# Optimization experiments

Hardware: AMD Instinct MI355X
Metric: run time of the kernel (lower is better)

Reference implementation:

```python
import jax, jax.numpy as jnp
import numpy as np

GRID_SIZE = 5
SPLINE_ORDER = 3
NUM_EXPERTS = 8
TOP_K = 2
CAP_FACTOR = 1.25
TEMP = 1.0
GDHW = (4, 4, 4)


def make_grid(in_features):
    # efficient-KAN grid buffer: grid_range=[-1,1], extended by spline_order on each side
    h = 2.0 / GRID_SIZE
    g = jnp.arange(-SPLINE_ORDER, GRID_SIZE + SPLINE_ORDER + 1, dtype=jnp.float32) * h - 1.0
    return jnp.broadcast_to(g, (in_features, g.shape[0]))


def b_splines(x, grid):
    # x: (N, in) -> (N, in, GRID_SIZE + SPLINE_ORDER) Cox-de Boor bases
    x = x[:, :, None]
    bases = ((x >= grid[:, :-1]) & (x < grid[:, 1:])).astype(x.dtype)
    for k in range(1, SPLINE_ORDER + 1):
        left = (x - grid[:, : -(k + 1)]) / (grid[:, k:-1] - grid[:, : -(k + 1)])
        right = (grid[:, k + 1:] - x) / (grid[:, k + 1:] - grid[:, 1:-k])
        bases = left * bases[:, :, :-1] + right * bases[:, :, 1:]
    return bases


def kan_linear(x, base_w, spline_w, scaler, grid):
    base = jax.nn.silu(x) @ base_w.T
    bs = b_splines(x, grid)                                   # (N, in, coef)
    spline = jnp.einsum('nic,oic->no', bs, spline_w * scaler[:, :, None])
    return base + spline


def layernorm(x, w, b, eps=1e-5):
    mu = x.mean(-1, keepdims=True)
    var = x.var(-1, keepdims=True)
    return (x - mu) / jnp.sqrt(var + eps) * w + b


def setup_inputs() -> dict:
    key = jax.random.key(0)
    ks = jax.random.split(key, 12)
    Cf, hidden, E, nc = 256, 170, NUM_EXPERTS, 2
    coef = GRID_SIZE + SPLINE_ORDER
    def nrm(k, shape, scale):
        return jax.random.normal(k, shape, dtype=jnp.float32) * scale
    return {
        'fpn_feat': nrm(ks[0], (8, 254, 32, 32, 32), 1.0),
        'seg_logits': nrm(ks[1], (8, 2, 32, 32, 32), 1.0),
        'ln_r_w': jnp.ones((Cf,), jnp.float32),
        'ln_r_b': jnp.zeros((Cf,), jnp.float32),
        'ln_h_w': jnp.ones((Cf,), jnp.float32),
        'ln_h_b': jnp.zeros((Cf,), jnp.float32),
        'router_w': nrm(ks[2], (E, Cf), Cf ** -0.5),
        'router_b': jnp.zeros((E,), jnp.float32),
        'bw1': nrm(ks[3], (E, hidden, Cf), Cf ** -0.5),
        'sw1': nrm(ks[4], (E, hidden, Cf, coef), 0.1 * Cf ** -0.5),
        'sc1': nrm(ks[5], (E, hidden, Cf), Cf ** -0.5),
        'bw2': nrm(ks[6], (E, Cf, hidden), hidden ** -0.5),
        'sw2': nrm(ks[7], (E, Cf, hidden, coef), 0.1 * hidden ** -0.5),
        'sc2': nrm(ks[8], (E, Cf, hidden), hidden ** -0.5),
        'cls_bw': nrm(ks[9], (nc, Cf), Cf ** -0.5),
        'cls_sw': nrm(ks[10], (nc, Cf, coef), 0.1 * Cf ** -0.5),
        'cls_sc': nrm(ks[11], (nc, Cf), Cf ** -0.5),
        'grid_cf': make_grid(Cf),
        'grid_hid': make_grid(hidden),
    }


def reference(fpn_feat, seg_logits, ln_r_w, ln_r_b, ln_h_w, ln_h_b,
              router_w, router_b, bw1, sw1, sc1, bw2, sw2, sc2,
              cls_bw, cls_sw, cls_sc, grid_cf, grid_hid):
    fused = jnp.concatenate([fpn_feat, seg_logits], axis=1)   # (B, Cf, D, H, W)
    B, C, D, H, W = fused.shape
    gd, gh, gw = GDHW
    dp, hp, wp = D // gd, H // gh, W // gw
    # split into gd*gh*gw blocks per sample
    blk = fused.reshape(B, C, gd, dp, gh, hp, gw, wp)
    blk = blk.transpose(0, 2, 4, 6, 1, 3, 5, 7).reshape(-1, C, dp, hp, wp)
    vec = blk.mean(axis=(2, 3, 4))                            # (N, Cf) global avg pool

    N = vec.shape[0]
    E = NUM_EXPERTS
    x_norm = layernorm(vec, ln_r_w, ln_r_b)
    scores = (x_norm @ router_w.T + router_b) / TEMP          # (N, E)
    top_val, top_idx = jax.lax.top_k(scores, TOP_K)
    top_w = jax.nn.softmax(top_val, axis=-1)
    capacity = int(CAP_FACTOR * N * TOP_K / E) + 1

    onehot = top_idx[None] == jnp.arange(E)[:, None, None]    # (E, N, K)
    sel = onehot.any(-1)                                      # (E, N)
    pos = jnp.cumsum(sel.astype(jnp.int32), axis=1)           # rank among selected (1-based)
    keep = sel & (pos <= capacity)                            # capacity drop = first-come order
    w = (top_w[None] * onehot.astype(top_w.dtype)).sum(-1)    # (E, N) combine weights

    def expert(bw1e, sw1e, sc1e, bw2e, sw2e, sc2e):
        h = kan_linear(x_norm, bw1e, sw1e, sc1e, grid_cf)
        h = jax.nn.gelu(h, approximate=False)                 # torch nn.GELU default (erf)
        return kan_linear(h, bw2e, sw2e, sc2e, grid_hid)

    y_all = jax.vmap(expert)(bw1, sw1, sc1, bw2, sw2, sc2)    # (E, N, Cf)
    out = jnp.einsum('en,enc->nc', keep.astype(vec.dtype) * w, y_all)

    conf = scores.max(-1)                                     # (N,)
    logits_blk = kan_linear(layernorm(out, ln_h_w, ln_h_b), cls_bw, cls_sw, cls_sc, grid_cf)
    P = gd * gh * gw
    weight = jax.nn.softmax(conf.reshape(B, P), axis=-1)[:, :, None]
    logits = (logits_blk.reshape(B, P, -1) * weight).sum(1)   # (B, num_classes)
    return logits
```

## Files before the change

kernel.cpp:

```cpp
#include <hip/hip_runtime.h>
#include <math.h>

#define CF 256
#define HID 170
#define NE 8
#define NTOK 512
#define K1 2304
#define K2P 1536
#define CAPACITY 161

typedef __bf16 bf16x8 __attribute__((ext_vector_type(8)));
typedef unsigned short u16x8 __attribute__((ext_vector_type(8)));
typedef float f32x4 __attribute__((ext_vector_type(4)));

__device__ __forceinline__ float silu_f(float x) { return x / (1.0f + expf(-x)); }
__device__ __forceinline__ float gelu_f(float x) {
    return 0.5f * x * (1.0f + erff(x * 0.70710678118654752f));
}

__device__ __forceinline__ unsigned short f2bf(float f) {
    unsigned int u = __float_as_uint(f);
    u = u + 0x7fffu + ((u >> 16) & 1u);
    return (unsigned short)(u >> 16);
}

__device__ __forceinline__ void bspline8(float x, float bs[8]) {
    float b[11];
#pragma unroll
    for (int j = 0; j < 11; ++j) {
        float g0 = (float)(j - 3) * 0.4f - 1.0f;
        float g1 = (float)(j - 2) * 0.4f - 1.0f;
        b[j] = (x >= g0 && x < g1) ? 1.0f : 0.0f;
    }
#pragma unroll
    for (int k = 1; k <= 3; ++k) {
        float inv = 2.5f / (float)k;
#pragma unroll
        for (int j = 0; j < 10 - (k - 1); ++j) {
            float gj   = (float)(j - 3) * 0.4f - 1.0f;
            float gjk1 = (float)(j - 2 + k) * 0.4f - 1.0f;
            b[j] = (x - gj) * inv * b[j] + (gjk1 - x) * inv * b[j + 1];
        }
    }
#pragma unroll
    for (int c = 0; c < 8; ++c) bs[c] = b[c];
}

__global__ __launch_bounds__(256) void mega_front_kernel(const float* __restrict__ fpn,
                                                         const float* __restrict__ seg,
                                                         const float* __restrict__ bw1,
                                                         const float* __restrict__ sw1,
                                                         const float* __restrict__ sc1,
                                                         const float* __restrict__ bw2,
                                                         const float* __restrict__ sw2,
                                                         const float* __restrict__ sc2,
                                                         float* __restrict__ vec,
                                                         unsigned short* __restrict__ W1,
                                                         unsigned short* __restrict__ W2) {
    int id = blockIdx.x, tid = threadIdx.x;
    if (id < 2048) {
        int c = id & 255, b = id >> 8;
        const float* src = (c < 254) ? fpn + (size_t)(b * 254 + c) * 32768
                                     : seg + (size_t)(b * 2 + (c - 254)) * 32768;
        const float4* s4 = (const float4*)src;
        float s[4] = {0.f, 0.f, 0.f, 0.f};
#pragma unroll
        for (int it = 0; it < 32; ++it) {
            float4 v = s4[it * 256 + tid];
            s[it >> 3] += v.x + v.y + v.z + v.w;
        }
        __shared__ float acc[64];
        if (tid < 64) acc[tid] = 0.0f;
        __syncthreads();
        int bh = tid >> 6, bw = (tid & 7) >> 1;
#pragma unroll
        for (int bd = 0; bd < 4; ++bd) atomicAdd(&acc[bd * 16 + bh * 4 + bw], s[bd]);
        __syncthreads();
        if (tid < 64) vec[(size_t)(b * 64 + tid) * CF + c] = acc[tid] * (1.0f / 512.0f);
    } else if (id < 2048 + NE * HID) {
        int r = id - 2048;
        int o = r % HID, e = r / HID, i = tid;
        size_t oi = (size_t)(e * HID + o) * CF + i;
        unsigned short* row = W1 + (size_t)(e * HID + o) * K1;
        row[i] = f2bf(bw1[oi]);
        float sc = sc1[oi];
        const float* sw = sw1 + oi * 8;
        u16x8 pk;
#pragma unroll
        for (int c = 0; c < 8; ++c) pk[c] = f2bf(sw[c] * sc);
        *(u16x8*)(row + CF + i * 8) = pk;
    } else {
        int r = id - (2048 + NE * HID);
        int o = r & 255, e = r >> 8, t = tid;
        unsigned short* row = W2 + (size_t)(e * CF + o) * K2P;
        if (t < HID) {
            size_t oi = (size_t)(e * CF + o) * HID + t;
            row[t] = f2bf(bw2[oi]);
            float sc = sc2[oi];
            const float* sw = sw2 + oi * 8;
            u16x8 pk;
#pragma unroll
            for (int c = 0; c < 8; ++c) pk[c] = f2bf(sw[c] * sc);
            *(u16x8*)(row + HID + t * 8) = pk;
        } else if (t < HID + 6) {
            row[HID * 9 + (t - HID)] = 0;
        }
    }
}

__global__ __launch_bounds__(256) void ln_score_a1_kernel(const float* __restrict__ vec,
                                                          const float* __restrict__ lnw,
                                                          const float* __restrict__ lnb,
                                                          const float* __restrict__ rw,
                                                          const float* __restrict__ rb,
                                                          float* __restrict__ scores,
                                                          unsigned short* __restrict__ A1) {
    int n = blockIdx.x, i = threadIdx.x;
    float v = vec[(size_t)n * CF + i];
    float s1 = v, s2 = v * v;
#pragma unroll
    for (int off = 32; off > 0; off >>= 1) {
        s1 += __shfl_xor(s1, off);
        s2 += __shfl_xor(s2, off);
    }
    __shared__ float rs1[4], rs2[4];
    int lane = i & 63, wid = i >> 6;
    if (lane == 0) { rs1[wid] = s1; rs2[wid] = s2; }
    __syncthreads();
    float tot1 = rs1[0] + rs1[1] + rs1[2] + rs1[3];
    float tot2 = rs2[0] + rs2[1] + rs2[2] + rs2[3];
    float mu = tot1 * (1.0f / CF);
    float var = tot2 * (1.0f / CF) - mu * mu;
    float rsd = rsqrtf(var + 1e-5f);
    float xv = (v - mu) * rsd * lnw[i] + lnb[i];
    unsigned short* r = A1 + (size_t)n * K1;
    r[i] = f2bf(silu_f(xv));
    float bs[8]; bspline8(xv, bs);
    u16x8 pk;
#pragma unroll
    for (int c = 0; c < 8; ++c) pk[c] = f2bf(bs[c]);
    *(u16x8*)(r + CF + i * 8) = pk;
    float p[NE];
#pragma unroll
    for (int e = 0; e < NE; ++e) p[e] = xv * rw[e * CF + i];
#pragma unroll
    for (int off = 32; off > 0; off >>= 1)
#pragma unroll
        for (int e = 0; e < NE; ++e) p[e] += __shfl_xor(p[e], off);
    __shared__ float pacc[4][NE];
    if (lane == 0)
#pragma unroll
        for (int e = 0; e < NE; ++e) pacc[wid][e] = p[e];
    __syncthreads();
    if (i < NE)
        scores[n * NE + i] = pacc[0][i] + pacc[1][i] + pacc[2][i] + pacc[3][i] + rb[i];
}

__global__ __launch_bounds__(512) void topk_kernel(const float* __restrict__ scores,
                                                   float* __restrict__ cw,
                                                   float* __restrict__ conf) {
    int n = threadIdx.x;
    __shared__ int   ti0[NTOK], ti1[NTOK];
    __shared__ float tw0[NTOK], tw1[NTOK];
    float m1 = -1e30f, m2 = -1e30f; int i1 = 0, i2 = 0;
#pragma unroll
    for (int e = 0; e < NE; ++e) {
        float sc = scores[n * NE + e];
        if (sc > m1) { m2 = m1; i2 = i1; m1 = sc; i1 = e; }
        else if (sc > m2) { m2 = sc; i2 = e; }
    }
    conf[n] = m1;
    float ew = expf(m2 - m1);
    ti0[n] = i1; ti1[n] = i2;
    tw0[n] = 1.0f / (1.0f + ew); tw1[n] = ew / (1.0f + ew);
    __syncthreads();
    int e = n >> 6, lane = n & 63;
    int cnt = 0;
    for (int c = 0; c < NTOK / 64; ++c) {
        int t = c * 64 + lane;
        int h0 = (ti0[t] == e), h1 = (ti1[t] == e);
        int sel = h0 | h1;
        unsigned long long mask = __ballot(sel);
        int pos = cnt + (int)__popcll(mask & ((1ull << lane) - 1ull));
        float wv = 0.f;
        if (sel && pos < CAPACITY) wv = h0 ? tw0[t] : tw1[t];
        cw[e * NTOK + t] = wv;
        cnt += (int)__popcll(mask);
    }
}

__global__ __launch_bounds__(256) void gemm_mfma_kernel(const unsigned short* __restrict__ Ag,
                                                        const unsigned short* __restrict__ Bg,
                                                        float* __restrict__ C,
                                                        unsigned short* __restrict__ A2,
                                                        int N, int K, long sA, long sB, long sC,
                                                        int ldc, int mode) {
    int e = blockIdx.z;
    const unsigned short* A = Ag + (size_t)e * sA;
    const unsigned short* B = Bg + (size_t)e * sB;
    int m0 = blockIdx.y * 64, n0 = blockIdx.x * 64;

    __shared__ alignas(16) unsigned char AsB[8192];
    __shared__ alignas(16) unsigned char BsB[8192];

    int tid = threadIdx.x;
    int lane = tid & 63, w = tid >> 6;
    int wr = w >> 1, wc = w & 1;
    int fr = lane & 15, fg = lane >> 4;
    int srow = tid >> 3;
    int schunk = tid & 7;

    int r0 = srow, r1 = srow + 32;
    int wb0 = r0 * 128 + ((schunk * 16) ^ ((r0 & 7) << 4));
    int wb1 = r1 * 128 + ((schunk * 16) ^ ((r1 & 7) << 4));

    f32x4 acc[2][2];
#pragma unroll
    for (int i = 0; i < 2; ++i)
#pragma unroll
        for (int j = 0; j < 2; ++j)
#pragma unroll
            for (int r = 0; r < 4; ++r) acc[i][j][r] = 0.f;

    int bn0 = n0 + r0, bn1 = n0 + r1;
    const int steps = K >> 6;
    u16x8 a0, a1, b0, b1;
    a0 = *(const u16x8*)(A + (size_t)(m0 + r0) * K + schunk * 8);
    a1 = *(const u16x8*)(A + (size_t)(m0 + r1) * K + schunk * 8);
    b0 = b1 = (u16x8){0, 0, 0, 0, 0, 0, 0, 0};
    if (bn0 < N) b0 = *(const u16x8*)(B + (size_t)bn0 * K + schunk * 8);
    if (bn1 < N) b1 = *(const u16x8*)(B + (size_t)bn1 * K + schunk * 8);

    for (int s = 0; s < steps; ++s) {
        __syncthreads();
        *(u16x8*)(AsB + wb0) = a0;
        *(u16x8*)(AsB + wb1) = a1;
        *(u16x8*)(BsB + wb0) = b0;
        *(u16x8*)(BsB + wb1) = b1;
        __syncthreads();
        if (s + 1 < steps) {
            int k0 = (s + 1) << 6;
            a0 = *(const u16x8*)(A + (size_t)(m0 + r0) * K + k0 + schunk * 8);
            a1 = *(const u16x8*)(A + (size_t)(m0 + r1) * K + k0 + schunk * 8);
            if (bn0 < N) b0 = *(const u16x8*)(B + (size_t)bn0 * K + k0 + schunk * 8);
            if (bn1 < N) b1 = *(const u16x8*)(B + (size_t)bn1 * K + k0 + schunk * 8);
        }
#pragma unroll
        for (int ks = 0; ks < 2; ++ks) {
            int kb = ks * 64 + fg * 16;
            u16x8 af[2], bf[2];
#pragma unroll
            for (int mf = 0; mf < 2; ++mf) {
                int row = wr * 32 + mf * 16 + fr;
                af[mf] = *(const u16x8*)(AsB + row * 128 + (kb ^ ((row & 7) << 4)));
            }
#pragma unroll
            for (int nf = 0; nf < 2; ++nf) {
                int row = wc * 32 + nf * 16 + fr;
                bf[nf] = *(const u16x8*)(BsB + row * 128 + (kb ^ ((row & 7) << 4)));
            }
#pragma unroll
            for (int mf = 0; mf < 2; ++mf)
#pragma unroll
                for (int nf = 0; nf < 2; ++nf)
                    acc[mf][nf] = __builtin_amdgcn_mfma_f32_16x16x32_bf16(
                        __builtin_bit_cast(bf16x8, af[mf]),
                        __builtin_bit_cast(bf16x8, bf[nf]), acc[mf][nf], 0, 0, 0);
        }
    }

    if (mode == 1) {
#pragma unroll
        for (int mf = 0; mf < 2; ++mf)
#pragma unroll
            for (int nf = 0; nf < 2; ++nf)
#pragma unroll
                for (int r = 0; r < 4; ++r) {
                    int row = m0 + wr * 32 + mf * 16 + fg * 4 + r;
                    int col = n0 + wc * 32 + nf * 16 + fr;
                    if (col < N) {
                        float g = gelu_f(acc[mf][nf][r]);
                        unsigned short* rr = A2 + ((size_t)e * NTOK + row) * K2P;
                        rr[col] = f2bf(silu_f(g));
                        float bs[8]; bspline8(g, bs);
                        u16x8 pk;
#pragma unroll
                        for (int c = 0; c < 8; ++c) pk[c] = f2bf(bs[c]);
                        *(u16x8*)(rr + HID + col * 8) = pk;
                    }
                }
    } else {
        float* Ce = C + (size_t)e * sC;
#pragma unroll
        for (int mf = 0; mf < 2; ++mf)
#pragma unroll
            for (int nf = 0; nf < 2; ++nf)
#pragma unroll
                for (int r = 0; r < 4; ++r) {
                    int row = m0 + wr * 32 + mf * 16 + fg * 4 + r;
                    int col = n0 + wc * 32 + nf * 16 + fr;
                    if (col < N) Ce[(size_t)row * ldc + col] = acc[mf][nf][r];
                }
    }
}

__global__ __launch_bounds__(256) void combcls_kernel(const float* __restrict__ y,
                                                      const float* __restrict__ cw,
                                                      const float* __restrict__ lnw,
                                                      const float* __restrict__ lnb,
                                                      const float* __restrict__ cbw,
                                                      const float* __restrict__ csw,
                                                      const float* __restrict__ csc,
                                                      float* __restrict__ lblk) {
    int n = blockIdx.x, i = threadIdx.x;
    float v = 0.f;
#pragma unroll
    for (int e = 0; e < NE; ++e)
        v += cw[e * NTOK + n] * y[((size_t)(e * NTOK + n)) * CF + i];
    float s1 = v, s2 = v * v;
#pragma unroll
    for (int off = 32; off > 0; off >>= 1) {
        s1 += __shfl_xor(s1, off);
        s2 += __shfl_xor(s2, off);
    }
    __shared__ float rA[4], rB[4], rP0[4], rP1[4];
    int lane = i & 63, wid = i >> 6;
    if (lane == 0) { rA[wid] = s1; rB[wid] = s2; }
    __syncthreads();
    float tot1 = rA[0] + rA[1] + rA[2] + rA[3];
    float tot2 = rB[0] + rB[1] + rB[2] + rB[3];
    float mu = tot1 * (1.0f / CF);
    float var = tot2 * (1.0f / CF) - mu * mu;
    float rs = rsqrtf(var + 1e-5f);
    float xh = (v - mu) * rs * lnw[i] + lnb[i];
    float si = silu_f(xh);
    float bs[8]; bspline8(xh, bs);
    float p0 = si * cbw[i], p1 = si * cbw[CF + i];
    float sp0 = 0.f, sp1 = 0.f;
#pragma unroll
    for (int c = 0; c < 8; ++c) {
        sp0 += bs[c] * csw[(size_t)i * 8 + c];
        sp1 += bs[c] * csw[(size_t)(CF + i) * 8 + c];
    }
    p0 += sp0 * csc[i];
    p1 += sp1 * csc[CF + i];
#pragma unroll
    for (int off = 32; off > 0; off >>= 1) {
        p0 += __shfl_xor(p0, off);
        p1 += __shfl_xor(p1, off);
    }
    if (lane == 0) { rP0[wid] = p0; rP1[wid] = p1; }
    __syncthreads();
    if (i == 0) {
        lblk[n * 2 + 0] = rP0[0] + rP0[1] + rP0[2] + rP0[3];
        lblk[n * 2 + 1] = rP1[0] + rP1[1] + rP1[2] + rP1[3];
    }
}

__global__ __launch_bounds__(64) void final_kernel(const float* __restrict__ conf,
                                                   const float* __restrict__ lblk,
                                                   float* __restrict__ out) {
    int b = blockIdx.x, p = threadIdx.x;
    float cf = conf[b * 64 + p];
    float mx = cf;
#pragma unroll
    for (int off = 32; off > 0; off >>= 1) mx = fmaxf(mx, __shfl_xor(mx, off));
    float ev = expf(cf - mx);
    float s = ev;
#pragma unroll
    for (int off = 32; off > 0; off >>= 1) s += __shfl_xor(s, off);
    float w = ev / s;
    float l0 = w * lblk[(b * 64 + p) * 2 + 0];
    float l1 = w * lblk[(b * 64 + p) * 2 + 1];
#pragma unroll
    for (int off = 32; off > 0; off >>= 1) {
        l0 += __shfl_xor(l0, off);
        l1 += __shfl_xor(l1, off);
    }
    if (p == 0) { out[b * 2 + 0] = l0; out[b * 2 + 1] = l1; }
}

extern "C" void kernel_launch(void* const* d_in, const int* in_sizes, int n_in,
                              void* d_out, int out_size, void* d_ws, size_t ws_size,
                              hipStream_t stream) {
    const float* fpn      = (const float*)d_in[0];
    const float* seg      = (const float*)d_in[1];
    const float* ln_r_w   = (const float*)d_in[2];
    const float* ln_r_b   = (const float*)d_in[3];
    const float* ln_h_w   = (const float*)d_in[4];
    const float* ln_h_b   = (const float*)d_in[5];
    const float* router_w = (const float*)d_in[6];
    const float* router_b = (const float*)d_in[7];
    const float* bw1      = (const float*)d_in[8];
    const float* sw1      = (const float*)d_in[9];
    const float* sc1      = (const float*)d_in[10];
    const float* bw2      = (const float*)d_in[11];
    const float* sw2      = (const float*)d_in[12];
    const float* sc2      = (const float*)d_in[13];
    const float* cls_bw   = (const float*)d_in[14];
    const float* cls_sw   = (const float*)d_in[15];
    const float* cls_sc   = (const float*)d_in[16];

    float* ws = (float*)d_ws;
    float* vec    = ws;
    float* scores = vec + 131072;
    float* cw     = scores + 4096;
    float* conf   = cw + 4096;
    float* lblk   = conf + 512;
    float* yall   = lblk + 1024;
    unsigned short* A1b = (unsigned short*)(yall + 1048576);
    unsigned short* W1b = A1b + (size_t)NTOK * K1;
    unsigned short* A2b = W1b + (size_t)NE * HID * K1;
    unsigned short* W2b = A2b + (size_t)NE * NTOK * K2P;

    mega_front_kernel<<<dim3(2048 + NE * HID + 2048), dim3(256), 0, stream>>>(
        fpn, seg, bw1, sw1, sc1, bw2, sw2, sc2, vec, W1b, W2b);
    ln_score_a1_kernel<<<dim3(NTOK), dim3(256), 0, stream>>>(vec, ln_r_w, ln_r_b, router_w,
                                                             router_b, scores, A1b);
    topk_kernel<<<dim3(1), dim3(512), 0, stream>>>(scores, cw, conf);
    gemm_mfma_kernel<<<dim3(3, 8, NE), dim3(256), 0, stream>>>(
        A1b, W1b, nullptr, A2b, HID, K1, 0L, (long)HID * K1, 0L, 0, 1);
    gemm_mfma_kernel<<<dim3(4, 8, NE), dim3(256), 0, stream>>>(
        A2b, W2b, yall, nullptr, CF, K2P, (long)NTOK * K2P, (long)CF * K2P,
        (long)NTOK * CF, CF, 0);
    combcls_kernel<<<dim3(NTOK), dim3(256), 0, stream>>>(yall, cw, ln_h_w, ln_h_b, cls_bw,
                                                         cls_sw, cls_sc, lblk);
    final_kernel<<<dim3(8), dim3(64), 0, stream>>>(conf, lblk, (float*)d_out);
}
```

Measured before the change: 117.1 us.

## Use direct global-to-LDS double-buffered loads in GEMM and fuse small kernels

The GEMM mainloop now stages tiles with global_load_lds into double-buffered shared memory, waiting on vmcnt, instead of loading through registers and storing to LDS. The top-k routing kernel is folded into an extra block of the first GEMM launch, and the final softmax-weighted reduction moves into combcls using atomicAdd into an output zeroed by the front kernel. This removes two launches and register staging, at the cost of atomic ordering nondeterminism and the removal of the N-bound guard on B loads, which now reads rows beyond N into padded tiles.

```diff
diff --git a/kernel.cpp b/kernel.cpp
--- a/kernel.cpp
+++ b/kernel.cpp
@@ -22,6 +22,12 @@
     unsigned int u = __float_as_uint(f);
     u = u + 0x7fffu + ((u >> 16) & 1u);
     return (unsigned short)(u >> 16);
+}
+
+__device__ __forceinline__ void gl_lds16(const unsigned short* g, unsigned short* l) {
+    __builtin_amdgcn_global_load_lds(
+        (const __attribute__((address_space(1))) unsigned int*)g,
+        (__attribute__((address_space(3))) unsigned int*)l, 16, 0, 0);
 }
 
 __device__ __forceinline__ void bspline8(float x, float bs[8]) {
@@ -56,8 +62,10 @@
                                                          const float* __restrict__ sc2,
                                                          float* __restrict__ vec,
                                                          unsigned short* __restrict__ W1,
-                                                         unsigned short* __restrict__ W2) {
+                                                         unsigned short* __restrict__ W2,
+                                                         float* __restrict__ out) {
     int id = blockIdx.x, tid = threadIdx.x;
+    if (id == 2048 && tid < 16) out[tid] = 0.0f;
     if (id < 2048) {
         int c = id & 255, b = id >> 8;
         const float* src = (c < 254) ? fpn + (size_t)(b * 254 + c) * 32768
@@ -114,8 +122,13 @@
                                                           const float* __restrict__ rw,
                                                           const float* __restrict__ rb,
                                                           float* __restrict__ scores,
-                                                          unsigned short* __restrict__ A1) {
+                                                          unsigned short* __restrict__ A1,
+                                                          unsigned short* __restrict__ A2) {
     int n = blockIdx.x, i = threadIdx.x;
+    if (i < 48) {
+        int e = i / 6, j = i - e * 6;
+        A2[((size_t)e * NTOK + n) * K2P + HID * 9 + j] = 0;
+    }
     float v = vec[(size_t)n * CF + i];
     float s1 = v, s2 = v * v;
 #pragma unroll
@@ -156,63 +169,80 @@
         scores[n * NE + i] = pacc[0][i] + pacc[1][i] + pacc[2][i] + pacc[3][i] + rb[i];
 }
 
-__global__ __launch_bounds__(512) void topk_kernel(const float* __restrict__ scores,
-                                                   float* __restrict__ cw,
-                                                   float* __restrict__ conf) {
-    int n = threadIdx.x;
+__global__ __launch_bounds__(256) void gemm_mfma_kernel(
+        const unsigned short* __restrict__ Ag, const unsigned short* __restrict__ Bg,
+        float* __restrict__ C, unsigned short* __restrict__ A2,
+        const float* __restrict__ scores, float* __restrict__ cw, float* __restrict__ conf,
+        int N, int K, long sA, long sB, long sC, int ldc, int mode) {
+    __shared__ alignas(16) unsigned short As[2][4096];
+    __shared__ alignas(16) unsigned short Bs[2][4096];
     __shared__ int   ti0[NTOK], ti1[NTOK];
     __shared__ float tw0[NTOK], tw1[NTOK];
-    float m1 = -1e30f, m2 = -1e30f; int i1 = 0, i2 = 0;
-#pragma unroll
-    for (int e = 0; e < NE; ++e) {
-        float sc = scores[n * NE + e];
-        if (sc > m1) { m2 = m1; i2 = i1; m1 = sc; i1 = e; }
-        else if (sc > m2) { m2 = sc; i2 = e; }
-    }
-    conf[n] = m1;
-    float ew = expf(m2 - m1);
-    ti0[n] = i1; ti1[n] = i2;
-    tw0[n] = 1.0f / (1.0f + ew); tw1[n] = ew / (1.0f + ew);
-    __syncthreads();
-    int e = n >> 6, lane = n & 63;
-    int cnt = 0;
-    for (int c = 0; c < NTOK / 64; ++c) {
-        int t = c * 64 + lane;
-        int h0 = (ti0[t] == e), h1 = (ti1[t] == e);
-        int sel = h0 | h1;
-        unsigned long long mask = __ballot(sel);
-        int pos = cnt + (int)__popcll(mask & ((1ull << lane) - 1ull));
-        float wv = 0.f;
-        if (sel && pos < CAPACITY) wv = h0 ? tw0[t] : tw1[t];
-        cw[e * NTOK + t] = wv;
-        cnt += (int)__popcll(mask);
-    }
-}
-
-__global__ __launch_bounds__(256) void gemm_mfma_kernel(const unsigned short* __restrict__ Ag,
-                                                        const unsigned short* __restrict__ Bg,
-                                                        float* __restrict__ C,
-                                                        unsigned short* __restrict__ A2,
-                                                        int N, int K, long sA, long sB, long sC,
-                                                        int ldc, int mode) {
+
+    int tid = threadIdx.x;
+    if (mode == 1 && blockIdx.x == 3) {
+        if (blockIdx.y != 0 || blockIdx.z != 0) return;
+        int lane = tid & 63, w4 = tid >> 6;
+#pragma unroll
+        for (int half = 0; half < 2; ++half) {
+            int n = half * 256 + tid;
+            float m1 = -1e30f, m2 = -1e30f; int i1 = 0, i2 = 0;
+#pragma unroll
+            for (int e = 0; e < NE; ++e) {
+                float sc = scores[n * NE + e];
+                if (sc > m1) { m2 = m1; i2 = i1; m1 = sc; i1 = e; }
+                else if (sc > m2) { m2 = sc; i2 = e; }
+            }
+            conf[n] = m1;
+            float ew = expf(m2 - m1);
+            ti0[n] = i1; ti1[n] = i2;
+            tw0[n] = 1.0f / (1.0f + ew); tw1[n] = ew / (1.0f + ew);
+        }
+        __syncthreads();
+#pragma unroll
+        for (int e2 = 0; e2 < 2; ++e2) {
+            int e = w4 * 2 + e2;
+            int cnt = 0;
+#pragma unroll
+            for (int c = 0; c < NTOK / 64; ++c) {
+                int t = c * 64 + lane;
+                int h0 = (ti0[t] == e), h1 = (ti1[t] == e);
+                int sel = h0 | h1;
+                unsigned long long mask = __ballot(sel);
+                int pos = cnt + (int)__popcll(mask & ((1ull << lane) - 1ull));
+                float wv = 0.f;
+                if (sel && pos < CAPACITY) wv = h0 ? tw0[t] : tw1[t];
+                cw[e * NTOK + t] = wv;
+                cnt += (int)__popcll(mask);
+            }
+        }
+        return;
+    }
+
     int e = blockIdx.z;
     const unsigned short* A = Ag + (size_t)e * sA;
     const unsigned short* B = Bg + (size_t)e * sB;
     int m0 = blockIdx.y * 64, n0 = blockIdx.x * 64;
-
-    __shared__ alignas(16) unsigned char AsB[8192];
-    __shared__ alignas(16) unsigned char BsB[8192];
-
-    int tid = threadIdx.x;
     int lane = tid & 63, w = tid >> 6;
     int wr = w >> 1, wc = w & 1;
     int fr = lane & 15, fg = lane >> 4;
-    int srow = tid >> 3;
-    int schunk = tid & 7;
-
-    int r0 = srow, r1 = srow + 32;
-    int wb0 = r0 * 128 + ((schunk * 16) ^ ((r0 & 7) << 4));
-    int wb1 = r1 * 128 + ((schunk * 16) ^ ((r1 & 7) << 4));
+    int lrow = lane >> 3, lch = lane & 7;
+    int csw = (lch ^ lrow) * 8;
+
+    const unsigned short* aS0 = A + (size_t)(m0 + w * 16 + lrow) * K + csw;
+    const unsigned short* aS1 = aS0 + (size_t)8 * K;
+    const unsigned short* bS0 = B + (size_t)(n0 + w * 16 + lrow) * K + csw;
+    const unsigned short* bS1 = bS0 + (size_t)8 * K;
+    unsigned short* dA0[2] = {&As[0][(w * 16) * 64], &As[1][(w * 16) * 64]};
+    unsigned short* dA1[2] = {&As[0][(w * 16 + 8) * 64], &As[1][(w * 16 + 8) * 64]};
+    unsigned short* dB0[2] = {&Bs[0][(w * 16) * 64], &Bs[1][(w * 16) * 64]};
+    unsigned short* dB1[2] = {&Bs[0][(w * 16 + 8) * 64], &Bs[1][(w * 16 + 8) * 64]};
+
+#define STAGE(bi, k0)                 \
+    gl_lds16(aS0 + (k0), dA0[bi]);    \
+    gl_lds16(aS1 + (k0), dA1[bi]);    \
+    gl_lds16(bS0 + (k0), dB0[bi]);    \
+    gl_lds16(bS1 + (k0), dB1[bi]);
 
     f32x4 acc[2][2];
 #pragma unroll
@@ -222,29 +252,20 @@
 #pragma unroll
             for (int r = 0; r < 4; ++r) acc[i][j][r] = 0.f;
 
-    int bn0 = n0 + r0, bn1 = n0 + r1;
     const int steps = K >> 6;
-    u16x8 a0, a1, b0, b1;
-    a0 = *(const u16x8*)(A + (size_t)(m0 + r0) * K + schunk * 8);
-    a1 = *(const u16x8*)(A + (size_t)(m0 + r1) * K + schunk * 8);
-    b0 = b1 = (u16x8){0, 0, 0, 0, 0, 0, 0, 0};
-    if (bn0 < N) b0 = *(const u16x8*)(B + (size_t)bn0 * K + schunk * 8);
-    if (bn1 < N) b1 = *(const u16x8*)(B + (size_t)bn1 * K + schunk * 8);
-
+    STAGE(0, 0);
     for (int s = 0; s < steps; ++s) {
-        __syncthreads();
-        *(u16x8*)(AsB + wb0) = a0;
-        *(u16x8*)(AsB + wb1) = a1;
-        *(u16x8*)(BsB + wb0) = b0;
-        *(u16x8*)(BsB + wb1) = b1;
-        __syncthreads();
+        int bi = s & 1;
         if (s + 1 < steps) {
-            int k0 = (s + 1) << 6;
-            a0 = *(const u16x8*)(A + (size_t)(m0 + r0) * K + k0 + schunk * 8);
-            a1 = *(const u16x8*)(A + (size_t)(m0 + r1) * K + k0 + schunk * 8);
-            if (bn0 < N) b0 = *(const u16x8*)(B + (size_t)bn0 * K + k0 + schunk * 8);
-            if (bn1 < N) b1 = *(const u16x8*)(B + (size_t)bn1 * K + k0 + schunk * 8);
-        }
+            STAGE(bi ^ 1, (s + 1) << 6);
+            asm volatile("s_waitcnt vmcnt(4)" ::: "memory");
+        } else {
+            asm volatile("s_waitcnt vmcnt(0)" ::: "memory");
+        }
+        __builtin_amdgcn_s_barrier();
+        asm volatile("" ::: "memory");
+        const unsigned char* Ab = (const unsigned char*)As[bi];
+        const unsigned char* Bb = (const unsigned char*)Bs[bi];
 #pragma unroll
         for (int ks = 0; ks < 2; ++ks) {
             int kb = ks * 64 + fg * 16;
@@ -252,12 +273,12 @@
 #pragma unroll
             for (int mf = 0; mf < 2; ++mf) {
                 int row = wr * 32 + mf * 16 + fr;
-                af[mf] = *(const u16x8*)(AsB + row * 128 + (kb ^ ((row & 7) << 4)));
+                af[mf] = *(const u16x8*)(Ab + row * 128 + (kb ^ ((row & 7) << 4)));
             }
 #pragma unroll
             for (int nf = 0; nf < 2; ++nf) {
                 int row = wc * 32 + nf * 16 + fr;
-                bf[nf] = *(const u16x8*)(BsB + row * 128 + (kb ^ ((row & 7) << 4)));
+                bf[nf] = *(const u16x8*)(Bb + row * 128 + (kb ^ ((row & 7) << 4)));
             }
 #pragma unroll
             for (int mf = 0; mf < 2; ++mf)
@@ -267,7 +288,11 @@
                         __builtin_bit_cast(bf16x8, af[mf]),
                         __builtin_bit_cast(bf16x8, bf[nf]), acc[mf][nf], 0, 0, 0);
         }
-    }
+        asm volatile("" ::: "memory");
+        __builtin_amdgcn_s_barrier();
+        asm volatile("" ::: "memory");
+    }
+#undef STAGE
 
     if (mode == 1) {
 #pragma unroll
@@ -306,12 +331,13 @@
 
 __global__ __launch_bounds__(256) void combcls_kernel(const float* __restrict__ y,
                                                       const float* __restrict__ cw,
+                                                      const float* __restrict__ conf,
                                                       const float* __restrict__ lnw,
                                                       const float* __restrict__ lnb,
                                                       const float* __restrict__ cbw,
                                                       const float* __restrict__ csw,
                                                       const float* __restrict__ csc,
-                                                      float* __restrict__ lblk) {
+                                                      float* __restrict__ out) {
     int n = blockIdx.x, i = threadIdx.x;
     float v = 0.f;
 #pragma unroll
@@ -351,33 +377,24 @@
     }
     if (lane == 0) { rP0[wid] = p0; rP1[wid] = p1; }
     __syncthreads();
-    if (i == 0) {
-        lblk[n * 2 + 0] = rP0[0] + rP0[1] + rP0[2] + rP0[3];
-        lblk[n * 2 + 1] = rP1[0] + rP1[1] + rP1[2] + rP1[3];
-    }
-}
-
-__global__ __launch_bounds__(64) void final_kernel(const float* __restrict__ conf,
-                                                   const float* __restrict__ lblk,
-                                                   float* __restrict__ out) {
-    int b = blockIdx.x, p = threadIdx.x;
-    float cf = conf[b * 64 + p];
-    float mx = cf;
-#pragma unroll
-    for (int off = 32; off > 0; off >>= 1) mx = fmaxf(mx, __shfl_xor(mx, off));
-    float ev = expf(cf - mx);
-    float s = ev;
-#pragma unroll
-    for (int off = 32; off > 0; off >>= 1) s += __shfl_xor(s, off);
-    float w = ev / s;
-    float l0 = w * lblk[(b * 64 + p) * 2 + 0];
-    float l1 = w * lblk[(b * 64 + p) * 2 + 1];
-#pragma unroll
-    for (int off = 32; off > 0; off >>= 1) {
-        l0 += __shfl_xor(l0, off);
-        l1 += __shfl_xor(l1, off);
-    }
-    if (p == 0) { out[b * 2 + 0] = l0; out[b * 2 + 1] = l1; }
+    if (i < 64) {
+        int b = n >> 6;
+        float cf = conf[b * 64 + i];
+        float mx = cf;
+#pragma unroll
+        for (int off = 32; off > 0; off >>= 1) mx = fmaxf(mx, __shfl_xor(mx, off));
+        float ev = expf(cf - mx);
+        float sum = ev;
+#pragma unroll
+        for (int off = 32; off > 0; off >>= 1) sum += __shfl_xor(sum, off);
+        if (i == 0) {
+            float wself = expf(conf[n] - mx) / sum;
+            float l0 = rP0[0] + rP0[1] + rP0[2] + rP0[3];
+            float l1 = rP1[0] + rP1[1] + rP1[2] + rP1[3];
+            atomicAdd(&out[b * 2 + 0], wself * l0);
+            atomicAdd(&out[b * 2 + 1], wself * l1);
+        }
+    }
 }
 
 extern "C" void kernel_launch(void* const* d_in, const int* in_sizes, int n_in,
@@ -400,30 +417,28 @@
     const float* cls_bw   = (const float*)d_in[14];
     const float* cls_sw   = (const float*)d_in[15];
     const float* cls_sc   = (const float*)d_in[16];
+    float* out = (float*)d_out;
 
     float* ws = (float*)d_ws;
     float* vec    = ws;
     float* scores = vec + 131072;
     float* cw     = scores + 4096;
     float* conf   = cw + 4096;
-    float* lblk   = conf + 512;
-    float* yall   = lblk + 1024;
+    float* yall   = conf + 512;
     unsigned short* A1b = (unsigned short*)(yall + 1048576);
     unsigned short* W1b = A1b + (size_t)NTOK * K1;
     unsigned short* A2b = W1b + (size_t)NE * HID * K1;
     unsigned short* W2b = A2b + (size_t)NE * NTOK * K2P;
 
     mega_front_kernel<<<dim3(2048 + NE * HID + 2048), dim3(256), 0, stream>>>(
-        fpn, seg, bw1, sw1, sc1, bw2, sw2, sc2, vec, W1b, W2b);
+        fpn, seg, bw1, sw1, sc1, bw2, sw2, sc2, vec, W1b, W2b, out);
     ln_score_a1_kernel<<<dim3(NTOK), dim3(256), 0, stream>>>(vec, ln_r_w, ln_r_b, router_w,
-                                                             router_b, scores, A1b);
-    topk_kernel<<<dim3(1), dim3(512), 0, stream>>>(scores, cw, conf);
-    gemm_mfma_kernel<<<dim3(3, 8, NE), dim3(256), 0, stream>>>(
-        A1b, W1b, nullptr, A2b, HID, K1, 0L, (long)HID * K1, 0L, 0, 1);
+                                                             router_b, scores, A1b, A2b);
     gemm_mfma_kernel<<<dim3(4, 8, NE), dim3(256), 0, stream>>>(
-        A2b, W2b, yall, nullptr, CF, K2P, (long)NTOK * K2P, (long)CF * K2P,
-        (long)NTOK * CF, CF, 0);
-    combcls_kernel<<<dim3(NTOK), dim3(256), 0, stream>>>(yall, cw, ln_h_w, ln_h_b, cls_bw,
-                                                         cls_sw, cls_sc, lblk);
-    final_kernel<<<dim3(8), dim3(64), 0, stream>>>(conf, lblk, (float*)d_out);
-}
+        A1b, W1b, nullptr, A2b, scores, cw, conf, HID, K1, 0L, (long)HID * K1, 0L, 0, 1);
+    gemm_mfma_kernel<<<dim3(4, 8, NE), dim3(256), 0, stream>>>(
+        A2b, W2b, yall, nullptr, nullptr, nullptr, nullptr, CF, K2P, (long)NTOK * K2P,
+        (long)CF * K2P, (long)NTOK * CF, CF, 0);
+    combcls_kernel<<<dim3(NTOK), dim3(256), 0, stream>>>(yall, cw, conf, ln_h_w, ln_h_b,
+                                                         cls_bw, cls_sw, cls_sc, out);
+}
```

Result: slower. 133.3 us (+13.8%).
